# Performance work log

Measured on AMD Instinct MI355X. Metric: run time of the kernel, lower is better.

Reference implementation:

```python
import jax, jax.numpy as jnp
import numpy as np
from jax import lax

B, N, D, S, K = 8, 4096, 61, 1024, 32
MLP = (64, 64, 128)
WN = (3, 8, 8, 16)  # WeightNet: 3 -> 8 -> 8 -> 16
EPS = 1e-5


def _gather(p, idx):
    # p: [B, N, C], idx: [B, ...] -> [B, ..., C]
    return jax.vmap(lambda pb, ib: pb[ib])(p, idx)


def _fps(xyz, npoint, key):
    # farthest point sampling, xyz: [B, N, 3] -> idx [B, npoint]
    b, n, _ = xyz.shape
    start = jax.random.randint(key, (b,), 0, n)
    def step(carry, _):
        dmin, far = carry
        centroid = jnp.take_along_axis(xyz, far[:, None, None], axis=1)  # [B,1,3]
        d = jnp.sum((xyz - centroid) ** 2, -1)                            # [B,N]
        dmin = jnp.minimum(dmin, d)
        return (dmin, jnp.argmax(dmin, -1)), far
    _, idxs = lax.scan(step, (jnp.full((b, n), 1e10, xyz.dtype), start), None, length=npoint)
    return idxs.T  # [B, npoint]


def _sqdist(a, b):
    # a: [B,S,3], b: [B,N,3] -> [B,S,N]
    return (jnp.sum(a ** 2, -1)[:, :, None] + jnp.sum(b ** 2, -1)[:, None, :]
            - 2.0 * jnp.einsum('bsc,bnc->bsn', a, b))


def _bn_relu(x, g, be):
    # channels-last BN (training-mode batch stats, biased var) + ReLU
    axes = tuple(range(x.ndim - 1))
    m = x.mean(axes, keepdims=True)
    v = x.var(axes, keepdims=True)
    return jax.nn.relu(g * (x - m) * lax.rsqrt(v + EPS) + be)


def _forward(xyz, points, mlp_p, wn_p, lin_w, lin_b, bnl_g, bnl_b):
    xyz_t = xyz.transpose(0, 2, 1)    # [B,N,3]
    pts = points.transpose(0, 2, 1)   # [B,N,D]
    xyz_sg = lax.stop_gradient(xyz_t)  # index computations carry no grads (as in torch)
    fps_idx = _fps(xyz_sg, S, jax.random.key(42))  # [B,S]
    new_xyz = _gather(xyz_t, fps_idx)              # [B,S,3]
    idx = lax.top_k(-_sqdist(lax.stop_gradient(new_xyz), xyz_sg), K)[1]  # [B,S,K]
    g_norm = _gather(xyz_t, idx) - new_xyz[:, :, None, :]                # [B,S,K,3]
    feat = jnp.concatenate([g_norm, _gather(pts, idx)], -1)              # [B,S,K,3+D]
    for w, b, g, be in mlp_p:
        feat = _bn_relu(jnp.einsum('bskc,oc->bsko', feat, w) + b, g, be)
    wts = g_norm
    for w, b, g, be in wn_p:
        wts = _bn_relu(jnp.einsum('bskc,oc->bsko', wts, w) + b, g, be)   # [B,S,K,16]
    # [B,S,C,K] @ [B,S,K,16] -> [B,S,C,16] -> [B,S,C*16] (C-major flatten, as torch .view)
    agg = jnp.einsum('bskc,bskw->bscw', feat, wts).reshape(B, S, -1)
    out = agg @ lin_w.T + lin_b                                          # [B,S,128]
    m = out.mean((0, 1), keepdims=True)  # BatchNorm1d over batch and spatial
    v = out.var((0, 1), keepdims=True)
    out = jax.nn.relu(bnl_g * (out - m) * lax.rsqrt(v + EPS) + bnl_b)
    return new_xyz.transpose(0, 2, 1), out.transpose(0, 2, 1)  # [B,3,S], [B,128,S]


def setup_inputs() -> dict:
    key = jax.random.key(0)
    ks = iter(jax.random.split(key, 64))
    inp = {"xyz": jax.random.normal(next(ks), (B, 3, N), jnp.float32),
           "points": jax.random.normal(next(ks), (B, D, N), jnp.float32)}
    mlp_in = (3 + D,) + MLP[:-1]
    for i, (ci, co) in enumerate(zip(mlp_in, MLP)):
        inp[f"mlp_w{i}"] = jax.random.normal(next(ks), (co, ci), jnp.float32) / np.float32(np.sqrt(ci))
        inp[f"mlp_b{i}"] = jnp.zeros((co,), jnp.float32)
        inp[f"mlp_g{i}"] = jnp.ones((co,), jnp.float32)
        inp[f"mlp_be{i}"] = jnp.zeros((co,), jnp.float32)
    for i, (ci, co) in enumerate(zip(WN[:-1], WN[1:])):
        inp[f"wn_w{i}"] = jax.random.normal(next(ks), (co, ci), jnp.float32) / np.float32(np.sqrt(ci))
        inp[f"wn_b{i}"] = jnp.zeros((co,), jnp.float32)
        inp[f"wn_g{i}"] = jnp.ones((co,), jnp.float32)
        inp[f"wn_be{i}"] = jnp.zeros((co,), jnp.float32)
    fin = 16 * MLP[-1]
    inp["lin_w"] = jax.random.normal(next(ks), (MLP[-1], fin), jnp.float32) / np.float32(np.sqrt(fin))
    inp["lin_b"] = jnp.zeros((MLP[-1],), jnp.float32)
    inp["bnl_g"] = jnp.ones((MLP[-1],), jnp.float32)
    inp["bnl_b"] = jnp.zeros((MLP[-1],), jnp.float32)
    return inp


def reference(xyz, points, mlp_w0, mlp_b0, mlp_g0, mlp_be0, mlp_w1, mlp_b1, mlp_g1, mlp_be1, mlp_w2, mlp_b2, mlp_g2, mlp_be2, wn_w0, wn_b0, wn_g0, wn_be0, wn_w1, wn_b1, wn_g1, wn_be1, wn_w2, wn_b2, wn_g2, wn_be2, lin_w, lin_b, bnl_g, bnl_b):
    mlp_p = [(mlp_w0, mlp_b0, mlp_g0, mlp_be0),
             (mlp_w1, mlp_b1, mlp_g1, mlp_be1),
             (mlp_w2, mlp_b2, mlp_g2, mlp_be2)]
    wn_p = [(wn_w0, wn_b0, wn_g0, wn_be0),
            (wn_w1, wn_b1, wn_g1, wn_be1),
            (wn_w2, wn_b2, wn_g2, wn_be2)]
    return _forward(xyz, points, mlp_p, wn_p, lin_w, lin_b, bnl_g, bnl_b)
```

## Files before the change

### kernel.cpp

```cpp
#include <hip/hip_runtime.h>
#include <cstdint>
#include <cstddef>


constexpr int B_ = 8, N_ = 4096, D_ = 61, S_ = 1024, K_ = 32;
constexpr int P_ = B_ * S_ * K_;
constexpr int BS_ = B_ * S_;

constexpr size_t OFF_STATS  = 0;
constexpr size_t OFF_NEWXYZ = 8192;
constexpr size_t OFF_KNN    = 106496;
constexpr size_t OFF_PT     = 1155072;
constexpr size_t OFF_Y01    = 9543680;
constexpr size_t OFF_Y2     = 76652544;
constexpr size_t OFF_W01    = 210870272;
constexpr size_t OFF_W2B    = 219258880;
constexpr size_t OFF_OUTPRE = OFF_W01;

static inline uint32_t rotl32(uint32_t x, int r){ return (x << r) | (x >> (32 - r)); }
static void tf2x32(uint32_t k0, uint32_t k1, uint32_t x0, uint32_t x1,
                   uint32_t* o0, uint32_t* o1){
  uint32_t ks[3] = {k0, k1, k0 ^ k1 ^ 0x1BD11BDAu};
  x0 += ks[0]; x1 += ks[1];
  const int RA[4] = {13,15,26,6}, RB[4] = {17,29,16,24};
  for (int i = 0; i < 5; ++i){
    const int* R = (i & 1) ? RB : RA;
    for (int j = 0; j < 4; ++j){ x0 += x1; x1 = rotl32(x1, R[j]); x1 ^= x0; }
    x0 += ks[(i+1)%3]; x1 += ks[(i+2)%3] + (uint32_t)(i+1);
  }
  *o0 = x0; *o1 = x1;
}
struct StartIdx { int v[8]; };
static StartIdx compute_starts(){
  uint32_t ka, kb;
  tf2x32(0u, 42u, 0u, 1u, &ka, &kb);
  StartIdx s;
  for (int i = 0; i < 8; ++i){
    uint32_t b1, b2;
    tf2x32(ka, kb, 0u, (uint32_t)i, &b1, &b2);
    s.v[i] = (int)((b1 ^ b2) & 4095u);
  }
  return s;
}

template<int C>
__device__ __forceinline__ unsigned long long dpp_max_u64_step(unsigned long long k){
  unsigned lo = (unsigned)k, hi = (unsigned)(k >> 32);
  unsigned olo = (unsigned)__builtin_amdgcn_update_dpp(0, (int)lo, C, 0xf, 0xf, true);
  unsigned ohi = (unsigned)__builtin_amdgcn_update_dpp(0, (int)hi, C, 0xf, 0xf, true);
  unsigned long long o = ((unsigned long long)ohi << 32) | olo;
  return o > k ? o : k;
}
__device__ __forceinline__ unsigned long long dpp_wave_max_u64(unsigned long long k){
  k = dpp_max_u64_step<0x111>(k);
  k = dpp_max_u64_step<0x112>(k);
  k = dpp_max_u64_step<0x114>(k);
  k = dpp_max_u64_step<0x118>(k);
  k = dpp_max_u64_step<0x142>(k);
  k = dpp_max_u64_step<0x143>(k);
  return k;
}
template<int C>
__device__ __forceinline__ unsigned long long dpp_min_u64_step(unsigned long long k){
  unsigned lo = (unsigned)k, hi = (unsigned)(k >> 32);
  unsigned olo = (unsigned)__builtin_amdgcn_update_dpp(-1, (int)lo, C, 0xf, 0xf, false);
  unsigned ohi = (unsigned)__builtin_amdgcn_update_dpp(-1, (int)hi, C, 0xf, 0xf, false);
  unsigned long long o = ((unsigned long long)ohi << 32) | olo;
  return o < k ? o : k;
}
__device__ __forceinline__ unsigned long long dpp_wave_min_u64(unsigned long long k){
  k = dpp_min_u64_step<0x111>(k);
  k = dpp_min_u64_step<0x112>(k);
  k = dpp_min_u64_step<0x114>(k);
  k = dpp_min_u64_step<0x118>(k);
  k = dpp_min_u64_step<0x142>(k);
  k = dpp_min_u64_step<0x143>(k);
  unsigned lo = (unsigned)__builtin_amdgcn_readlane((int)(unsigned)k, 63);
  unsigned hi = (unsigned)__builtin_amdgcn_readlane((int)(unsigned)(k >> 32), 63);
  return ((unsigned long long)hi << 32) | lo;
}
template<int C>
__device__ __forceinline__ float dpp_add_step(float x){
  int t = __builtin_amdgcn_update_dpp(0, (int)__float_as_uint(x), C, 0xf, 0xf, true);
  return x + __uint_as_float((unsigned)t);
}
__device__ __forceinline__ float dpp_row_sum16(float x){
  x = dpp_add_step<0x111>(x);
  x = dpp_add_step<0x112>(x);
  x = dpp_add_step<0x114>(x);
  x = dpp_add_step<0x118>(x);
  return x;
}
__device__ __forceinline__ unsigned ordf(float f){
  unsigned u = __float_as_uint(f);
  return u ^ (unsigned)(((int)u >> 31) | 0x80000000);
}
__device__ __forceinline__ void atomAddD(double* p, double v){
  __hip_atomic_fetch_add(p, v, __ATOMIC_RELAXED, __HIP_MEMORY_SCOPE_AGENT);
}

#define REP8(M) M(0) M(1) M(2) M(3) M(4) M(5) M(6) M(7)

__global__ __launch_bounds__(512, 1) void fps_tr_kernel(const float* __restrict__ xyz,
                                                        const float* __restrict__ pts,
                                                        StartIdx st,
                                                        float* __restrict__ new_xyz,
                                                        float* __restrict__ out_xyz,
                                                        float* __restrict__ pT){
  __shared__ float4 pts4[N_];
  __shared__ unsigned short win[S_];
  __shared__ unsigned long long slots[2][8];
  const int tid = threadIdx.x;

  if (blockIdx.x >= 8){
    float* tile = (float*)pts4;
    const int tt = blockIdx.x - 8;
    const int b = tt >> 6, n0 = (tt & 63) * 64;
    for (int e = tid; e < 61*64; e += 512){
      int d = e >> 6, c = e & 63;
      tile[d*65 + c] = pts[((size_t)b*61 + d)*N_ + n0 + c];
    }
    __syncthreads();
    for (int e = tid; e < 4096; e += 512){
      int r = e >> 6, d = e & 63;
      pT[((size_t)b*N_ + n0 + r)*64 + d] = (d < 61) ? tile[d*65 + r] : 0.f;
    }
    return;
  }

  const int b = blockIdx.x;
  const int lane = tid & 63, wv = tid >> 6;
  const float* xb = xyz + (size_t)b*3*N_;

#define LOADP(i) \
  float px##i = xb[tid + 512*(i)]; \
  float py##i = xb[N_ + tid + 512*(i)]; \
  float pz##i = xb[2*N_ + tid + 512*(i)]; \
  float dm##i = 1e10f; \
  const unsigned kl##i = ~(unsigned)(tid + 512*(i)); \
  pts4[tid + 512*(i)] = make_float4(px##i, py##i, pz##i, 0.f);
  REP8(LOADP)
#undef LOADP
  __syncthreads();

  int cur = st.v[b];
  float4 c4 = pts4[cur];
  float cx = c4.x, cy = c4.y, cz = c4.z;

  int par = 0;
  for (int s = 0; s < S_; ++s){
    if (tid == 0) win[s] = (unsigned short)cur;
    if (s == S_ - 1) break;
#define UPD(i) \
    unsigned long long key##i; { \
      float dx = __fsub_rn(px##i, cx), dy = __fsub_rn(py##i, cy), dz = __fsub_rn(pz##i, cz); \
      float d  = __fadd_rn(__fadd_rn(__fmul_rn(dx,dx), __fmul_rn(dy,dy)), __fmul_rn(dz,dz)); \
      dm##i = fminf(dm##i, d); \
      key##i = ((unsigned long long)__float_as_uint(dm##i) << 32) | kl##i; }
    REP8(UPD)
#undef UPD
    unsigned long long t0 = key0 > key1 ? key0 : key1;
    unsigned long long t1 = key2 > key3 ? key2 : key3;
    unsigned long long t2 = key4 > key5 ? key4 : key5;
    unsigned long long t3 = key6 > key7 ? key6 : key7;
    unsigned long long u0 = t0 > t1 ? t0 : t1;
    unsigned long long u1 = t2 > t3 ? t2 : t3;
    unsigned long long k  = u0 > u1 ? u0 : u1;
    k = dpp_wave_max_u64(k);
    if (lane == 63) slots[par][wv] = k;
    __syncthreads();
    unsigned long long bk = slots[par][0];
    { unsigned long long v1 = slots[par][1]; if (v1 > bk) bk = v1;
      unsigned long long v2 = slots[par][2]; if (v2 > bk) bk = v2;
      unsigned long long v3 = slots[par][3]; if (v3 > bk) bk = v3;
      unsigned long long v4 = slots[par][4]; if (v4 > bk) bk = v4;
      unsigned long long v5 = slots[par][5]; if (v5 > bk) bk = v5;
      unsigned long long v6 = slots[par][6]; if (v6 > bk) bk = v6;
      unsigned long long v7 = slots[par][7]; if (v7 > bk) bk = v7; }
    cur = (int)(~(unsigned)bk) & (N_ - 1);
    float4 w4 = pts4[cur];
    cx = w4.x; cy = w4.y; cz = w4.z;
    par ^= 1;
  }
  __syncthreads();
  for (int s2 = tid; s2 < S_; s2 += 512){
    float4 p = pts4[win[s2]];
    new_xyz[((size_t)b*S_ + s2)*3 + 0] = p.x;
    new_xyz[((size_t)b*S_ + s2)*3 + 1] = p.y;
    new_xyz[((size_t)b*S_ + s2)*3 + 2] = p.z;
    out_xyz[(size_t)b*3*S_ + s2]        = p.x;
    out_xyz[(size_t)b*3*S_ + S_ + s2]   = p.y;
    out_xyz[(size_t)b*3*S_ + 2*S_ + s2] = p.z;
  }
}
#undef REP8

__global__ __launch_bounds__(256) void knn_kernel(const float* __restrict__ xyz,
                                                  const float* __restrict__ nxyz,
                                                  int* __restrict__ knn_idx){
  __shared__ float dist[4][4096];
  const int wv = threadIdx.x >> 6, lane = threadIdx.x & 63;
  const int q = blockIdx.x*4 + wv;
  const int b = q >> 10;
  const float* xb = xyz + (size_t)b*3*N_;
  const float ax = nxyz[(size_t)q*3], ay = nxyz[(size_t)q*3+1], az = nxyz[(size_t)q*3+2];
  const float sa = __fadd_rn(__fadd_rn(__fmul_rn(ax,ax), __fmul_rn(ay,ay)), __fmul_rn(az,az));
  float* dw = dist[wv];
  unsigned long long kk = ~0ull;
  for (int i = 0; i < 64; ++i){
    int n = i*64 + lane;
    float x = xb[n], y = xb[N_+n], z = xb[2*N_+n];
    float sb  = __fadd_rn(__fadd_rn(__fmul_rn(x,x), __fmul_rn(y,y)), __fmul_rn(z,z));
    float dot = __fadd_rn(__fadd_rn(__fmul_rn(ax,x), __fmul_rn(ay,y)), __fmul_rn(az,z));
    float d   = __fsub_rn(__fadd_rn(sa, sb), __fmul_rn(2.f, dot));
    dw[i*64 + ((lane + i) & 63)] = d;
    unsigned long long key = ((unsigned long long)ordf(d) << 32) | (unsigned)n;
    if (key < kk) kk = key;
  }
  __syncthreads();
  int myout = 0;
  for (int r = 0; r < 32; ++r){
    unsigned long long g = dpp_wave_min_u64(kk);
    const int gn = (int)(g & 0xFFFFFFFFull);
    if (lane == r) myout = gn;
    const int col = gn & 63, row = gn >> 6;
    const int a = lane*64 + ((col + lane) & 63);
    float v = dw[a];
    if (lane == row){ v = 3.4e38f; dw[a] = 3.4e38f; }
    unsigned long long nk = ((unsigned long long)ordf(v) << 32)
                          | (unsigned)(lane*64 + col);
    nk = dpp_wave_min_u64(nk);
    if (lane == col) kk = nk;
  }
  if (lane < 32) knn_idx[(size_t)q*32 + lane] = myout;
}

__device__ __forceinline__ void bn_coeff(const double* st, const float* g, const float* be,
                                         int c, double cnt, float* sc, float* sh){
  double mean = st[c*2] / cnt;
  double var  = st[c*2+1] / cnt - mean*mean;
  double scale = (double)g[c] / sqrt(var + 1e-5);
  *sc = (float)scale; *sh = (float)((double)be[c] - mean*scale);
}

#define STATS64(ACC_EXPR, ST, CH_OFF)                                          \
  {                                                                            \
    _Pragma("unroll")                                                          \
    for (int o = 0; o < 64; ++o){                                              \
      float v_ = (ACC_EXPR);                                                   \
      float s1_ = dpp_row_sum16(v_);                                           \
      float q1_ = dpp_row_sum16(v_*v_);                                        \
      if ((threadIdx.x & 15) == 15){                                           \
        int rid_ = threadIdx.x >> 4;                                           \
        redS[rid_][o] = s1_; redQ[rid_][o] = q1_;                              \
      }                                                                        \
    }                                                                          \
    __syncthreads();                                                           \
    if (threadIdx.x < 64){                                                     \
      float s_ = 0.f;                                                          \
      _Pragma("unroll")                                                        \
      for (int r_ = 0; r_ < 16; ++r_) s_ += redS[r_][threadIdx.x];             \
      atomAddD(&(ST)[((CH_OFF) + threadIdx.x)*2], (double)s_);                 \
    } else if (threadIdx.x < 128){                                             \
      int o_ = threadIdx.x - 64;                                               \
      float s_ = 0.f;                                                          \
      _Pragma("unroll")                                                        \
      for (int r_ = 0; r_ < 16; ++r_) s_ += redQ[r_][o_];                      \
      atomAddD(&(ST)[((CH_OFF) + o_)*2 + 1], (double)s_);                      \
    }                                                                          \
  }

__global__ __launch_bounds__(256, 2) void m0_kernel(const float* __restrict__ pT,
                                                    const float* __restrict__ xyz,
                                                    const float* __restrict__ nxyz,
                                                    const int* __restrict__ knn_idx,
                                                    const float* __restrict__ w,
                                                    const float* __restrict__ bias,
                                                    float* __restrict__ y,
                                                    double* __restrict__ stout){
  __shared__ float Wt[4096]; __shared__ float bb[64];
  __shared__ float redS[16][65], redQ[16][65];
  for (int t = threadIdx.x; t < 4096; t += 256){ int o = t >> 6, c = t & 63; Wt[c*64+o] = w[o*64+c]; }
  if (threadIdx.x < 64) bb[threadIdx.x] = bias[threadIdx.x];
  __syncthreads();
  const int p = blockIdx.x*256 + threadIdx.x;
  const int b = p >> 15, s = (p & 32767) >> 5;
  const int n = knn_idx[p];
  float in[64];
  {
    const float* xb = xyz + (size_t)b*3*N_;
    const int q = (b << 10) + s;
    in[0] = xb[n]       - nxyz[(size_t)q*3];
    in[1] = xb[N_+n]    - nxyz[(size_t)q*3+1];
    in[2] = xb[2*N_+n]  - nxyz[(size_t)q*3+2];
    const float* pr = pT + ((size_t)b*N_ + n)*64;
#pragma unroll
    for (int d = 0; d < 60; d += 4){
      float4 v = *reinterpret_cast<const float4*>(&pr[d]);
      in[3+d] = v.x; in[4+d] = v.y; in[5+d] = v.z; in[6+d] = v.w;
    }
    in[63] = pr[60];
  }
  float acc[64];
#pragma unroll
  for (int o = 0; o < 64; ++o) acc[o] = bb[o];
#pragma unroll
  for (int c = 0; c < 64; ++c){
    float x = in[c];
#pragma unroll
    for (int o = 0; o < 64; o += 4){
      float4 w4 = *reinterpret_cast<const float4*>(&Wt[c*64+o]);
      acc[o]   += x*w4.x; acc[o+1] += x*w4.y; acc[o+2] += x*w4.z; acc[o+3] += x*w4.w;
    }
  }
#pragma unroll
  for (int o = 0; o < 64; ++o) y[(size_t)o*P_ + p] = acc[o];
  STATS64(acc[o], stout, 0)
}

__global__ __launch_bounds__(256, 2) void m1_kernel(float* __restrict__ y,
                                                    const float* __restrict__ w,
                                                    const float* __restrict__ bias,
                                                    const double* __restrict__ stin,
                                                    const float* __restrict__ g,
                                                    const float* __restrict__ be,
                                                    double* __restrict__ stout){
  __shared__ float Wt[4096]; __shared__ float bb[64], sc[64], sh[64];
  __shared__ float redS[16][65], redQ[16][65];
  for (int t = threadIdx.x; t < 4096; t += 256){ int o = t >> 6, c = t & 63; Wt[c*64+o] = w[o*64+c]; }
  if (threadIdx.x < 64){
    bn_coeff(stin, g, be, threadIdx.x, (double)P_, &sc[threadIdx.x], &sh[threadIdx.x]);
    bb[threadIdx.x] = bias[threadIdx.x];
  }
  __syncthreads();
  const int p = blockIdx.x*256 + threadIdx.x;
  float in[64];
#pragma unroll
  for (int c = 0; c < 64; ++c){
    float x = y[(size_t)c*P_ + p];
    in[c] = fmaxf(0.f, fmaf(x, sc[c], sh[c]));
  }
  float acc[64];
#pragma unroll
  for (int o = 0; o < 64; ++o) acc[o] = bb[o];
#pragma unroll
  for (int c = 0; c < 64; ++c){
    float x = in[c];
#pragma unroll
    for (int o = 0; o < 64; o += 4){
      float4 w4 = *reinterpret_cast<const float4*>(&Wt[c*64+o]);
      acc[o]   += x*w4.x; acc[o+1] += x*w4.y; acc[o+2] += x*w4.z; acc[o+3] += x*w4.w;
    }
  }
#pragma unroll
  for (int o = 0; o < 64; ++o) y[(size_t)o*P_ + p] = acc[o];
  STATS64(acc[o], stout, 0)
}

__global__ __launch_bounds__(256, 2) void m2_kernel(const float* __restrict__ y1,
                                                    float* __restrict__ y2,
                                                    const float* __restrict__ w,
                                                    const float* __restrict__ bias,
                                                    const double* __restrict__ stin,
                                                    const float* __restrict__ g,
                                                    const float* __restrict__ be,
                                                    double* __restrict__ stout){
  __shared__ float Wt[4096]; __shared__ float bb[64], sc[64], sh[64];
  __shared__ float redS[16][65], redQ[16][65];
  const int half = blockIdx.y;
  for (int t = threadIdx.x; t < 4096; t += 256){
    int o = t >> 6, c = t & 63;
    Wt[c*64+o] = w[(size_t)(half*64+o)*64 + c];
  }
  if (threadIdx.x < 64){
    bn_coeff(stin, g, be, threadIdx.x, (double)P_, &sc[threadIdx.x], &sh[threadIdx.x]);
    bb[threadIdx.x] = bias[half*64 + threadIdx.x];
  }
  __syncthreads();
  const int p = blockIdx.x*256 + threadIdx.x;
  float in[64];
#pragma unroll
  for (int c = 0; c < 64; ++c){
    float x = y1[(size_t)c*P_ + p];
    in[c] = fmaxf(0.f, fmaf(x, sc[c], sh[c]));
  }
  float acc[64];
#pragma unroll
  for (int o = 0; o < 64; ++o) acc[o] = bb[o];
#pragma unroll
  for (int c = 0; c < 64; ++c){
    float x = in[c];
#pragma unroll
    for (int o = 0; o < 64; o += 4){
      float4 w4 = *reinterpret_cast<const float4*>(&Wt[c*64+o]);
      acc[o]   += x*w4.x; acc[o+1] += x*w4.y; acc[o+2] += x*w4.z; acc[o+3] += x*w4.w;
    }
  }
#pragma unroll
  for (int o = 0; o < 64; ++o) y2[(size_t)(half*64+o)*P_ + p] = acc[o];
  STATS64(acc[o], stout, half*64)
}

__global__ __launch_bounds__(256) void w0_kernel(const float* __restrict__ xyz,
                                                 const float* __restrict__ nxyz,
                                                 const int* __restrict__ knn_idx,
                                                 const float* __restrict__ w,
                                                 const float* __restrict__ bias,
                                                 float* __restrict__ wb,
                                                 double* __restrict__ stout){
  __shared__ float Wl[24], bb[8];
  __shared__ float redS[16][9], redQ[16][9];
  if (threadIdx.x < 24) Wl[threadIdx.x] = w[threadIdx.x];
  if (threadIdx.x < 8)  bb[threadIdx.x] = bias[threadIdx.x];
  __syncthreads();
  const int p = blockIdx.x*256 + threadIdx.x;
  const int b = p >> 15, s = (p & 32767) >> 5;
  const int n = knn_idx[p];
  const float* xb = xyz + (size_t)b*3*N_;
  const int q = (b << 10) + s;
  float gx = xb[n]      - nxyz[(size_t)q*3];
  float gy = xb[N_+n]   - nxyz[(size_t)q*3+1];
  float gz = xb[2*N_+n] - nxyz[(size_t)q*3+2];
  float a_[8];
#pragma unroll
  for (int o = 0; o < 8; ++o){
    a_[o] = bb[o] + gx*Wl[o*3] + gy*Wl[o*3+1] + gz*Wl[o*3+2];
    wb[(size_t)o*P_ + p] = a_[o];
  }
#pragma unroll
  for (int o = 0; o < 8; ++o){
    float s1 = dpp_row_sum16(a_[o]);
    float q1 = dpp_row_sum16(a_[o]*a_[o]);
    if ((threadIdx.x & 15) == 15){ int rid = threadIdx.x >> 4; redS[rid][o] = s1; redQ[rid][o] = q1; }
  }
  __syncthreads();
  if (threadIdx.x < 8){
    float s_ = 0.f;
#pragma unroll
    for (int r = 0; r < 16; ++r) s_ += redS[r][threadIdx.x];
    atomAddD(&stout[threadIdx.x*2], (double)s_);
  } else if (threadIdx.x < 16){
    int o = threadIdx.x - 8;
    float s_ = 0.f;
#pragma unroll
    for (int r = 0; r < 16; ++r) s_ += redQ[r][o];
    atomAddD(&stout[o*2+1], (double)s_);
  }
}

__global__ __launch_bounds__(256) void w1_kernel(float* __restrict__ wb,
                                                 const float* __restrict__ w,
                                                 const float* __restrict__ bias,
                                                 const double* __restrict__ stin,
                                                 const float* __restrict__ g,
                                                 const float* __restrict__ be,
                                                 double* __restrict__ stout){
  __shared__ float Wl[64], bb[8], sc[8], sh[8];
  __shared__ float redS[16][9], redQ[16][9];
  if (threadIdx.x < 64) Wl[threadIdx.x] = w[threadIdx.x];
  if (threadIdx.x < 8){
    bn_coeff(stin, g, be, threadIdx.x, (double)P_, &sc[threadIdx.x], &sh[threadIdx.x]);
    bb[threadIdx.x] = bias[threadIdx.x];
  }
  __syncthreads();
  const int p = blockIdx.x*256 + threadIdx.x;
  float in[8];
#pragma unroll
  for (int c = 0; c < 8; ++c){
    float x = wb[(size_t)c*P_ + p];
    in[c] = fmaxf(0.f, fmaf(x, sc[c], sh[c]));
  }
  float acc[8];
#pragma unroll
  for (int o = 0; o < 8; ++o){
    float a = bb[o];
#pragma unroll
    for (int c = 0; c < 8; ++c) a += in[c]*Wl[o*8+c];
    acc[o] = a;
  }
#pragma unroll
  for (int o = 0; o < 8; ++o) wb[(size_t)o*P_ + p] = acc[o];
#pragma unroll
  for (int o = 0; o < 8; ++o){
    float s1 = dpp_row_sum16(acc[o]);
    float q1 = dpp_row_sum16(acc[o]*acc[o]);
    if ((threadIdx.x & 15) == 15){ int rid = threadIdx.x >> 4; redS[rid][o] = s1; redQ[rid][o] = q1; }
  }
  __syncthreads();
  if (threadIdx.x < 8){
    float s_ = 0.f;
#pragma unroll
    for (int r = 0; r < 16; ++r) s_ += redS[r][threadIdx.x];
    atomAddD(&stout[threadIdx.x*2], (double)s_);
  } else if (threadIdx.x < 16){
    int o = threadIdx.x - 8;
    float s_ = 0.f;
#pragma unroll
    for (int r = 0; r < 16; ++r) s_ += redQ[r][o];
    atomAddD(&stout[o*2+1], (double)s_);
  }
}

__global__ __launch_bounds__(256) void w2_kernel(const float* __restrict__ wb,
                                                 float* __restrict__ wb2,
                                                 const float* __restrict__ w,
                                                 const float* __restrict__ bias,
                                                 const double* __restrict__ stin,
                                                 const float* __restrict__ g,
                                                 const float* __restrict__ be,
                                                 double* __restrict__ stout){
  __shared__ float Wl[128], bb[16], sc[8], sh[8];
  __shared__ float redS[16][17], redQ[16][17];
  if (threadIdx.x < 128) Wl[threadIdx.x] = w[threadIdx.x];
  if (threadIdx.x < 8)
    bn_coeff(stin, g, be, threadIdx.x, (double)P_, &sc[threadIdx.x], &sh[threadIdx.x]);
  if (threadIdx.x < 16) bb[threadIdx.x] = bias[threadIdx.x];
  __syncthreads();
  const int p = blockIdx.x*256 + threadIdx.x;
  float in[8];
#pragma unroll
  for (int c = 0; c < 8; ++c){
    float x = wb[(size_t)c*P_ + p];
    in[c] = fmaxf(0.f, fmaf(x, sc[c], sh[c]));
  }
  float acc[16];
#pragma unroll
  for (int o = 0; o < 16; ++o){
    float a = bb[o];
#pragma unroll
    for (int c = 0; c < 8; ++c) a += in[c]*Wl[o*8+c];
    acc[o] = a;
    wb2[(size_t)o*P_ + p] = a;
  }
#pragma unroll
  for (int o = 0; o < 16; ++o){
    float s1 = dpp_row_sum16(acc[o]);
    float q1 = dpp_row_sum16(acc[o]*acc[o]);
    if ((threadIdx.x & 15) == 15){ int rid = threadIdx.x >> 4; redS[rid][o] = s1; redQ[rid][o] = q1; }
  }
  __syncthreads();
  if (threadIdx.x < 16){
    float s_ = 0.f;
#pragma unroll
    for (int r = 0; r < 16; ++r) s_ += redS[r][threadIdx.x];
    atomAddD(&stout[threadIdx.x*2], (double)s_);
  } else if (threadIdx.x < 32){
    int o = threadIdx.x - 16;
    float s_ = 0.f;
#pragma unroll
    for (int r = 0; r < 16; ++r) s_ += redQ[r][o];
    atomAddD(&stout[o*2+1], (double)s_);
  }
}

__global__ __launch_bounds__(256) void agg_kernel(const float* __restrict__ y2,
                                                  const float* __restrict__ wb2,
                                                  const double* __restrict__ st2,
                                                  const float* __restrict__ g2,
                                                  const float* __restrict__ be2,
                                                  const double* __restrict__ stw,
                                                  const float* __restrict__ gw,
                                                  const float* __restrict__ bew,
                                                  float* __restrict__ agg){
  __shared__ float f[32*132];
  __shared__ float wt[32*16];
  __shared__ float sc2[128], sh2[128], scw[16], shw[16];
  const int t = threadIdx.x;
  if (t < 128) bn_coeff(st2, g2, be2, t, (double)P_, &sc2[t], &sh2[t]);
  if (t < 16)  bn_coeff(stw, gw, bew, t, (double)P_, &scw[t], &shw[t]);
  __syncthreads();
  const int bs = blockIdx.x;
  const size_t p0 = (size_t)bs * 32;
  for (int e = t; e < 4096; e += 256){
    int c = e >> 5, k = e & 31;
    float x = y2[(size_t)c*P_ + p0 + k];
    f[k*132 + c] = fmaxf(0.f, fmaf(x, sc2[c], sh2[c]));
  }
  for (int e = t; e < 512; e += 256){
    int w = e >> 5, k = e & 31;
    float x = wb2[(size_t)w*P_ + p0 + k];
    wt[k*16 + w] = fmaxf(0.f, fmaf(x, scw[w], shw[w]));
  }
  __syncthreads();
  const int c = t >> 1, wp = (t & 1) * 8;
  float a0=0,a1=0,a2=0,a3=0,a4=0,a5=0,a6=0,a7=0;
#pragma unroll
  for (int k = 0; k < 32; ++k){
    float fv = f[k*132 + c];
    float4 u = *reinterpret_cast<const float4*>(&wt[k*16 + wp]);
    float4 v = *reinterpret_cast<const float4*>(&wt[k*16 + wp + 4]);
    a0 += fv*u.x; a1 += fv*u.y; a2 += fv*u.z; a3 += fv*u.w;
    a4 += fv*v.x; a5 += fv*v.y; a6 += fv*v.z; a7 += fv*v.w;
  }
  float* dst = agg + (size_t)bs*2048 + c*16 + wp;
  *reinterpret_cast<float4*>(dst)     = make_float4(a0,a1,a2,a3);
  *reinterpret_cast<float4*>(dst + 4) = make_float4(a4,a5,a6,a7);
}

__global__ __launch_bounds__(256) void lin_kernel(const float* __restrict__ agg,
                                                  const float* __restrict__ lw,
                                                  const float* __restrict__ lb,
                                                  float* __restrict__ outp){
  __shared__ float A[32*33];
  __shared__ float Wl[32*128];
  __shared__ float lbs[128];
  const int t = threadIdx.x;
  const int r0 = blockIdx.x * 32;
  if (t < 128) lbs[t] = lb[t];
  const int c_lane = t & 31, rg = t >> 5;
  float acc[4][4];
#pragma unroll
  for (int i = 0; i < 4; ++i)
#pragma unroll
    for (int j = 0; j < 4; ++j) acc[i][j] = 0.f;

  for (int kk0 = 0; kk0 < 2048; kk0 += 32){
    __syncthreads();
    {
      int r = t >> 3, kq = (t & 7) * 4;
      float4 v = *reinterpret_cast<const float4*>(&agg[(size_t)(r0 + r)*2048 + kk0 + kq]);
      A[r*33 + kq]   = v.x; A[r*33 + kq+1] = v.y; A[r*33 + kq+2] = v.z; A[r*33 + kq+3] = v.w;
    }
    {
#pragma unroll
      for (int u = 0; u < 4; ++u){
        int fid = t + 256*u;
        int o = fid >> 3, kq = (fid & 7) * 4;
        float4 v = *reinterpret_cast<const float4*>(&lw[(size_t)o*2048 + kk0 + kq]);
        Wl[(kq  )*128 + o] = v.x; Wl[(kq+1)*128 + o] = v.y;
        Wl[(kq+2)*128 + o] = v.z; Wl[(kq+3)*128 + o] = v.w;
      }
    }
    __syncthreads();
#pragma unroll 8
    for (int kk = 0; kk < 32; ++kk){
      float a0 = A[(rg*4+0)*33 + kk], a1 = A[(rg*4+1)*33 + kk],
            a2 = A[(rg*4+2)*33 + kk], a3 = A[(rg*4+3)*33 + kk];
#pragma unroll
      for (int j = 0; j < 4; ++j){
        float wv = Wl[kk*128 + c_lane + 32*j];
        acc[0][j] += a0*wv; acc[1][j] += a1*wv; acc[2][j] += a2*wv; acc[3][j] += a3*wv;
      }
    }
  }
  __syncthreads();
#pragma unroll
  for (int i = 0; i < 4; ++i)
#pragma unroll
    for (int j = 0; j < 4; ++j){
      int o = c_lane + 32*j;
      outp[(size_t)(r0 + rg*4 + i)*128 + o] = acc[i][j] + lbs[o];
    }
}

__global__ __launch_bounds__(128) void statsF_kernel(const float* __restrict__ outp,
                                                     double* __restrict__ st){
  const int c = threadIdx.x;
  const int r0 = blockIdx.x * 128;
  double s = 0.0, q = 0.0;
  for (int r = 0; r < 128; ++r){
    double v = outp[(size_t)(r0 + r)*128 + c];
    s += v; q += v*v;
  }
  atomAddD(&st[c*2], s); atomAddD(&st[c*2+1], q);
}

__global__ __launch_bounds__(256) void final_kernel(const float* __restrict__ outp,
                                                    const double* __restrict__ st,
                                                    const float* __restrict__ g,
                                                    const float* __restrict__ be,
                                                    float* __restrict__ out){
  __shared__ float sc[128], sh[128];
  __shared__ float tile[64][129];
  const int t = threadIdx.x;
  if (t < 128) bn_coeff(st, g, be, t, (double)BS_, &sc[t], &sh[t]);
  const int bs0 = blockIdx.x * 64;
  const int b = bs0 >> 10, s0 = bs0 & 1023;
#pragma unroll
  for (int e = t; e < 8192; e += 256){
    int r = e >> 7, c = e & 127;
    tile[r][c] = outp[(size_t)(bs0 + r)*128 + c];
  }
  __syncthreads();
#pragma unroll
  for (int e = t; e < 8192; e += 256){
    int o = e >> 6, si = e & 63;
    float x = tile[si][o];
    out[(size_t)b*131072 + (size_t)o*1024 + s0 + si] = fmaxf(0.f, fmaf(x, sc[o], sh[o]));
  }
}

extern "C" void kernel_launch(void* const* d_in, const int* in_sizes, int n_in,
                              void* d_out, int out_size, void* d_ws, size_t ws_size,
                              hipStream_t stream){
  (void)in_sizes; (void)n_in; (void)out_size; (void)ws_size;
  const float* xyz    = (const float*)d_in[0];
  const float* points = (const float*)d_in[1];
  const float* mw0 = (const float*)d_in[2],  *mb0 = (const float*)d_in[3],
             * mg0 = (const float*)d_in[4],  *me0 = (const float*)d_in[5];
  const float* mw1 = (const float*)d_in[6],  *mb1 = (const float*)d_in[7],
             * mg1 = (const float*)d_in[8],  *me1 = (const float*)d_in[9];
  const float* mw2 = (const float*)d_in[10], *mb2 = (const float*)d_in[11],
             * mg2 = (const float*)d_in[12], *me2 = (const float*)d_in[13];
  const float* ww0 = (const float*)d_in[14], *wb0 = (const float*)d_in[15],
             * wg0 = (const float*)d_in[16], *we0 = (const float*)d_in[17];
  const float* ww1 = (const float*)d_in[18], *wb1 = (const float*)d_in[19],
             * wg1 = (const float*)d_in[20], *we1 = (const float*)d_in[21];
  const float* ww2 = (const float*)d_in[22], *wb2_ = (const float*)d_in[23],
             * wg2 = (const float*)d_in[24], *we2 = (const float*)d_in[25];
  const float* lw  = (const float*)d_in[26], *lb  = (const float*)d_in[27];
  const float* fg  = (const float*)d_in[28], *fb  = (const float*)d_in[29];

  char* ws = (char*)d_ws;
  double* ST0 = (double*)(ws + OFF_STATS);
  double* ST1 = (double*)(ws + OFF_STATS + 1024);
  double* ST2 = (double*)(ws + OFF_STATS + 2048);
  double* SW0 = (double*)(ws + OFF_STATS + 4096);
  double* SW1 = (double*)(ws + OFF_STATS + 4224);
  double* SW2 = (double*)(ws + OFF_STATS + 4352);
  double* STF = (double*)(ws + OFF_STATS + 4608);
  float* nxyz   = (float*)(ws + OFF_NEWXYZ);
  int*   knnidx = (int*)(ws + OFF_KNN);
  float* pT     = (float*)(ws + OFF_PT);
  float* y01    = (float*)(ws + OFF_Y01);
  float* y2     = (float*)(ws + OFF_Y2);
  float* w01    = (float*)(ws + OFF_W01);
  float* w2b    = (float*)(ws + OFF_W2B);
  float* aggbuf = (float*)(ws + OFF_Y01);
  float* outpre = (float*)(ws + OFF_OUTPRE);

  float* out_xyz  = (float*)d_out;
  float* out_feat = (float*)d_out + (size_t)B_*3*S_;

  hipMemsetAsync(ws + OFF_STATS, 0, 8192, stream);

  StartIdx st = compute_starts();
  fps_tr_kernel<<<dim3(8 + B_*64), dim3(512), 0, stream>>>(xyz, points, st, nxyz, out_xyz, pT);

  knn_kernel<<<dim3(BS_/4), dim3(256), 0, stream>>>(xyz, nxyz, knnidx);

  m0_kernel<<<dim3(P_/256), dim3(256), 0, stream>>>(pT, xyz, nxyz, knnidx, mw0, mb0, y01, ST0);
  m1_kernel<<<dim3(P_/256), dim3(256), 0, stream>>>(y01, mw1, mb1, ST0, mg0, me0, ST1);
  m2_kernel<<<dim3(P_/256, 2), dim3(256), 0, stream>>>(y01, y2, mw2, mb2, ST1, mg1, me1, ST2);

  w0_kernel<<<dim3(P_/256), dim3(256), 0, stream>>>(xyz, nxyz, knnidx, ww0, wb0, w01, SW0);
  w1_kernel<<<dim3(P_/256), dim3(256), 0, stream>>>(w01, ww1, wb1, SW0, wg0, we0, SW1);
  w2_kernel<<<dim3(P_/256), dim3(256), 0, stream>>>(w01, w2b, ww2, wb2_, SW1, wg1, we1, SW2);

  agg_kernel<<<dim3(BS_), dim3(256), 0, stream>>>(y2, w2b, ST2, mg2, me2, SW2, wg2, we2, aggbuf);
  lin_kernel<<<dim3(BS_/32), dim3(256), 0, stream>>>(aggbuf, lw, lb, outpre);
  statsF_kernel<<<dim3(BS_/128), dim3(128), 0, stream>>>(outpre, STF);
  final_kernel<<<dim3(BS_/64), dim3(256), 0, stream>>>(outpre, STF, fg, fb, out_feat);
}
```

Baseline: 1.543 ms.

## Restructure FPS argmax: 256 threads, f32 max then index min, carry winner coords

The farthest point sampling kernel drops from 512 to 256 threads, with each thread now holding 16 points instead of 8. The per-step argmax changes from a packed 64-bit key reduction to a 32-bit float max, followed by a 32-bit min over candidate indices. The winning thread writes its centroid coordinates into shared memory, so the LDS lookup by index is no longer needed after the barrier. This aims to cut per-iteration reduction cost and the cross-wave work on the serial critical path, at the cost of an extra wave reduction and more registers per thread.

```diff
diff --git a/kernel.cpp b/kernel.cpp
--- a/kernel.cpp
+++ b/kernel.cpp
@@ -44,21 +44,33 @@
 }
 
 template<int C>
-__device__ __forceinline__ unsigned long long dpp_max_u64_step(unsigned long long k){
-  unsigned lo = (unsigned)k, hi = (unsigned)(k >> 32);
-  unsigned olo = (unsigned)__builtin_amdgcn_update_dpp(0, (int)lo, C, 0xf, 0xf, true);
-  unsigned ohi = (unsigned)__builtin_amdgcn_update_dpp(0, (int)hi, C, 0xf, 0xf, true);
-  unsigned long long o = ((unsigned long long)ohi << 32) | olo;
-  return o > k ? o : k;
-}
-__device__ __forceinline__ unsigned long long dpp_wave_max_u64(unsigned long long k){
-  k = dpp_max_u64_step<0x111>(k);
-  k = dpp_max_u64_step<0x112>(k);
-  k = dpp_max_u64_step<0x114>(k);
-  k = dpp_max_u64_step<0x118>(k);
-  k = dpp_max_u64_step<0x142>(k);
-  k = dpp_max_u64_step<0x143>(k);
-  return k;
+__device__ __forceinline__ float dpp_max_f32_step(float x){
+  int t = __builtin_amdgcn_update_dpp(0, (int)__float_as_uint(x), C, 0xf, 0xf, true);
+  return fmaxf(x, __uint_as_float((unsigned)t));
+}
+__device__ __forceinline__ float dpp_wave_max_f32(float x){
+  x = dpp_max_f32_step<0x111>(x);
+  x = dpp_max_f32_step<0x112>(x);
+  x = dpp_max_f32_step<0x114>(x);
+  x = dpp_max_f32_step<0x118>(x);
+  x = dpp_max_f32_step<0x142>(x);
+  x = dpp_max_f32_step<0x143>(x);
+  return __uint_as_float((unsigned)__builtin_amdgcn_readlane((int)__float_as_uint(x), 63));
+}
+template<int C>
+__device__ __forceinline__ unsigned dpp_min_u32_step(unsigned x){
+  int t = __builtin_amdgcn_update_dpp(-1, (int)x, C, 0xf, 0xf, false);
+  unsigned u = (unsigned)t;
+  return u < x ? u : x;
+}
+__device__ __forceinline__ unsigned dpp_wave_min_u32(unsigned x){
+  x = dpp_min_u32_step<0x111>(x);
+  x = dpp_min_u32_step<0x112>(x);
+  x = dpp_min_u32_step<0x114>(x);
+  x = dpp_min_u32_step<0x118>(x);
+  x = dpp_min_u32_step<0x142>(x);
+  x = dpp_min_u32_step<0x143>(x);
+  return (unsigned)__builtin_amdgcn_readlane((int)x, 63);
 }
 template<int C>
 __device__ __forceinline__ unsigned long long dpp_min_u64_step(unsigned long long k){
@@ -99,9 +111,10 @@
   __hip_atomic_fetch_add(p, v, __ATOMIC_RELAXED, __HIP_MEMORY_SCOPE_AGENT);
 }
 
-#define REP8(M) M(0) M(1) M(2) M(3) M(4) M(5) M(6) M(7)
-
-__global__ __launch_bounds__(512, 1) void fps_tr_kernel(const float* __restrict__ xyz,
+#define REP16(M) M(0) M(1) M(2) M(3) M(4) M(5) M(6) M(7) \
+                 M(8) M(9) M(10) M(11) M(12) M(13) M(14) M(15)
+
+__global__ __launch_bounds__(256, 1) void fps_tr_kernel(const float* __restrict__ xyz,
                                                         const float* __restrict__ pts,
                                                         StartIdx st,
                                                         float* __restrict__ new_xyz,
@@ -109,19 +122,20 @@
                                                         float* __restrict__ pT){
   __shared__ float4 pts4[N_];
   __shared__ unsigned short win[S_];
-  __shared__ unsigned long long slots[2][8];
+  __shared__ unsigned long long slotK[2][4];
+  __shared__ float4 slotC[2][4];
   const int tid = threadIdx.x;
 
   if (blockIdx.x >= 8){
     float* tile = (float*)pts4;
     const int tt = blockIdx.x - 8;
     const int b = tt >> 6, n0 = (tt & 63) * 64;
-    for (int e = tid; e < 61*64; e += 512){
+    for (int e = tid; e < 61*64; e += 256){
       int d = e >> 6, c = e & 63;
       tile[d*65 + c] = pts[((size_t)b*61 + d)*N_ + n0 + c];
     }
     __syncthreads();
-    for (int e = tid; e < 4096; e += 512){
+    for (int e = tid; e < 4096; e += 256){
       int r = e >> 6, d = e & 63;
       pT[((size_t)b*N_ + n0 + r)*64 + d] = (d < 61) ? tile[d*65 + r] : 0.f;
     }
@@ -133,13 +147,12 @@
   const float* xb = xyz + (size_t)b*3*N_;
 
 #define LOADP(i) \
-  float px##i = xb[tid + 512*(i)]; \
-  float py##i = xb[N_ + tid + 512*(i)]; \
-  float pz##i = xb[2*N_ + tid + 512*(i)]; \
+  float px##i = xb[tid + 256*(i)]; \
+  float py##i = xb[N_ + tid + 256*(i)]; \
+  float pz##i = xb[2*N_ + tid + 256*(i)]; \
   float dm##i = 1e10f; \
-  const unsigned kl##i = ~(unsigned)(tid + 512*(i)); \
-  pts4[tid + 512*(i)] = make_float4(px##i, py##i, pz##i, 0.f);
-  REP8(LOADP)
+  pts4[tid + 256*(i)] = make_float4(px##i, py##i, pz##i, 0.f);
+  REP16(LOADP)
 #undef LOADP
   __syncthreads();
 
@@ -150,40 +163,58 @@
   int par = 0;
   for (int s = 0; s < S_; ++s){
     if (tid == 0) win[s] = (unsigned short)cur;
-    if (s == S_ - 1) break;
-#define UPD(i) \
-    unsigned long long key##i; { \
+#define UPD(i) { \
       float dx = __fsub_rn(px##i, cx), dy = __fsub_rn(py##i, cy), dz = __fsub_rn(pz##i, cz); \
       float d  = __fadd_rn(__fadd_rn(__fmul_rn(dx,dx), __fmul_rn(dy,dy)), __fmul_rn(dz,dz)); \
-      dm##i = fminf(dm##i, d); \
-      key##i = ((unsigned long long)__float_as_uint(dm##i) << 32) | kl##i; }
-    REP8(UPD)
+      dm##i = fminf(dm##i, d); }
+    REP16(UPD)
 #undef UPD
-    unsigned long long t0 = key0 > key1 ? key0 : key1;
-    unsigned long long t1 = key2 > key3 ? key2 : key3;
-    unsigned long long t2 = key4 > key5 ? key4 : key5;
-    unsigned long long t3 = key6 > key7 ? key6 : key7;
-    unsigned long long u0 = t0 > t1 ? t0 : t1;
-    unsigned long long u1 = t2 > t3 ? t2 : t3;
-    unsigned long long k  = u0 > u1 ? u0 : u1;
-    k = dpp_wave_max_u64(k);
-    if (lane == 63) slots[par][wv] = k;
+    float a0 = fmaxf(dm0, dm1),  a1 = fmaxf(dm2, dm3);
+    float a2 = fmaxf(dm4, dm5),  a3 = fmaxf(dm6, dm7);
+    float a4 = fmaxf(dm8, dm9),  a5 = fmaxf(dm10, dm11);
+    float a6 = fmaxf(dm12, dm13),a7 = fmaxf(dm14, dm15);
+    float b0 = fmaxf(a0, a1), b1 = fmaxf(a2, a3), b2 = fmaxf(a4, a5), b3 = fmaxf(a6, a7);
+    float lmax = fmaxf(fmaxf(b0, b1), fmaxf(b2, b3));
+    const float wmax = dpp_wave_max_f32(lmax);
+#define CANDI(i) unsigned c##i = (dm##i == wmax) ? (unsigned)(tid | ((i) << 8)) : 0xFFFFFFFFu;
+    REP16(CANDI)
+#undef CANDI
+    unsigned d0 = c0  < c1  ? c0  : c1,  d1 = c2  < c3  ? c2  : c3;
+    unsigned d2 = c4  < c5  ? c4  : c5,  d3 = c6  < c7  ? c6  : c7;
+    unsigned d4 = c8  < c9  ? c8  : c9,  d5 = c10 < c11 ? c10 : c11;
+    unsigned d6 = c12 < c13 ? c12 : c13, d7 = c14 < c15 ? c14 : c15;
+    unsigned e0 = d0 < d1 ? d0 : d1, e1 = d2 < d3 ? d2 : d3;
+    unsigned e2 = d4 < d5 ? d4 : d5, e3 = d6 < d7 ? d6 : d7;
+    unsigned f0 = e0 < e1 ? e0 : e1, f1 = e2 < e3 ? e2 : e3;
+    unsigned cand = f0 < f1 ? f0 : f1;
+    const unsigned widx = dpp_wave_min_u32(cand);
+    if (tid == (int)(widx & 255u)){
+      const int sl = (int)(widx >> 8);
+      float sx = px0, sy = py0, sz = pz0;
+#define SEL(i) if (sl == (i)){ sx = px##i; sy = py##i; sz = pz##i; }
+      SEL(1) SEL(2) SEL(3) SEL(4) SEL(5) SEL(6) SEL(7) SEL(8)
+      SEL(9) SEL(10) SEL(11) SEL(12) SEL(13) SEL(14) SEL(15)
+#undef SEL
+      slotK[par][wv] = ((unsigned long long)__float_as_uint(wmax) << 32)
+                     | (unsigned long long)(unsigned)(~widx);
+      slotC[par][wv] = make_float4(sx, sy, sz, 0.f);
+    }
     __syncthreads();
-    unsigned long long bk = slots[par][0];
-    { unsigned long long v1 = slots[par][1]; if (v1 > bk) bk = v1;
-      unsigned long long v2 = slots[par][2]; if (v2 > bk) bk = v2;
-      unsigned long long v3 = slots[par][3]; if (v3 > bk) bk = v3;
-      unsigned long long v4 = slots[par][4]; if (v4 > bk) bk = v4;
-      unsigned long long v5 = slots[par][5]; if (v5 > bk) bk = v5;
-      unsigned long long v6 = slots[par][6]; if (v6 > bk) bk = v6;
-      unsigned long long v7 = slots[par][7]; if (v7 > bk) bk = v7; }
-    cur = (int)(~(unsigned)bk) & (N_ - 1);
-    float4 w4 = pts4[cur];
-    cx = w4.x; cy = w4.y; cz = w4.z;
+    unsigned long long k0 = slotK[par][0], k1 = slotK[par][1],
+                       k2 = slotK[par][2], k3 = slotK[par][3];
+    float4 q0 = slotC[par][0], q1 = slotC[par][1],
+           q2 = slotC[par][2], q3 = slotC[par][3];
+    unsigned long long m0 = k0; float4 g0 = q0;
+    if (k1 > m0){ m0 = k1; g0 = q1; }
+    unsigned long long m1 = k2; float4 g1 = q2;
+    if (k3 > m1){ m1 = k3; g1 = q3; }
+    if (m1 > m0){ m0 = m1; g0 = g1; }
+    cur = (int)(~(unsigned)m0) & (N_ - 1);
+    cx = g0.x; cy = g0.y; cz = g0.z;
     par ^= 1;
   }
   __syncthreads();
-  for (int s2 = tid; s2 < S_; s2 += 512){
+  for (int s2 = tid; s2 < S_; s2 += 256){
     float4 p = pts4[win[s2]];
     new_xyz[((size_t)b*S_ + s2)*3 + 0] = p.x;
     new_xyz[((size_t)b*S_ + s2)*3 + 1] = p.y;
@@ -193,7 +224,7 @@
     out_xyz[(size_t)b*3*S_ + 2*S_ + s2] = p.z;
   }
 }
-#undef REP8
+#undef REP16
 
 __global__ __launch_bounds__(256) void knn_kernel(const float* __restrict__ xyz,
                                                   const float* __restrict__ nxyz,
@@ -735,7 +766,7 @@
   hipMemsetAsync(ws + OFF_STATS, 0, 8192, stream);
 
   StartIdx st = compute_starts();
-  fps_tr_kernel<<<dim3(8 + B_*64), dim3(512), 0, stream>>>(xyz, points, st, nxyz, out_xyz, pT);
+  fps_tr_kernel<<<dim3(8 + B_*64), dim3(256), 0, stream>>>(xyz, points, st, nxyz, out_xyz, pT);
 
   knn_kernel<<<dim3(BS_/4), dim3(256), 0, stream>>>(xyz, nxyz, knnidx);
 
```

After: 1.772 ms. 1.15x slower.
